# Optimization experiments

Measured on AMD Instinct MI355X. Metric: run time of the kernel, lower is better.

## Reference

```python
import jax, jax.numpy as jnp
import numpy as np

T, B, D, H, R, S, M = 1024, 16, 512, 8, 32, 16, 16
TQ = R + T + S   # query length
KL = M + R + T   # key/value length
NEG_INF = -1e8


def setup_inputs() -> dict:
    key = jax.random.key(0)
    ks = jax.random.split(key, 12)
    utterance = jax.random.normal(ks[0], (T, B, D), jnp.float32)
    right_context = jax.random.normal(ks[1], (R, B, D), jnp.float32)
    summary = jax.random.normal(ks[2], (S, B, D), jnp.float32)
    mems = jax.random.normal(ks[3], (M, B, D), jnp.float32)
    # valid lengths in [T//2, T]; force max == T so data-dependent shapes are static
    lengths = jax.random.randint(ks[4], (B,), T // 2, T + 1).at[0].set(T).astype(jnp.int64)
    # block-streaming style mask: query i may only attend to keys <= i + M
    q_idx = jnp.arange(TQ)[:, None]
    k_idx = jnp.arange(KL)[None, :]
    attention_mask = k_idx > (q_idx + M)  # True = masked
    scale = 0.02
    Wq = jax.random.normal(ks[5], (D, D), jnp.float32) * scale
    bq = jnp.zeros((D,), jnp.float32)
    Wkv = jax.random.normal(ks[6], (2 * D, D), jnp.float32) * scale
    bkv = jnp.zeros((2 * D,), jnp.float32)
    Wo = jax.random.normal(ks[7], (D, D), jnp.float32) * scale
    bo = jnp.zeros((D,), jnp.float32)
    return dict(utterance=utterance, lengths=lengths, right_context=right_context,
                summary=summary, mems=mems, attention_mask=attention_mask,
                Wq=Wq, bq=bq, Wkv=Wkv, bkv=bkv, Wo=Wo, bo=bo)


def _split_heads(x):
    # (L, B, D) -> (B*H, L, D//H), matching torch .view(-1, B*H, d).transpose(0, 1)
    L = x.shape[0]
    return x.reshape(L, B * H, D // H).transpose(1, 0, 2)


def reference(utterance, lengths, right_context, summary, mems, attention_mask,
              Wq, bq, Wkv, bkv, Wo, bo):
    d_head = D // H
    scaling = d_head ** -0.5

    query_in = jnp.concatenate([right_context, utterance, summary], axis=0)   # (TQ, B, D)
    kv_in = jnp.concatenate([mems, right_context, utterance], axis=0)         # (KL, B, D)

    query = query_in @ Wq.T + bq
    kv = kv_in @ Wkv.T + bkv
    k, v = jnp.split(kv, 2, axis=2)

    q = _split_heads(query)  # (B*H, TQ, d)
    kh = _split_heads(k)     # (B*H, KL, d)
    vh = _split_heads(v)

    w = jnp.einsum('nqd,nkd->nqk', q * scaling, kh).astype(jnp.float32)
    w = jnp.where(attention_mask[None, :, :], NEG_INF, w)

    # padding mask (B > 1 path): klengths = lengths + M + right_context_blocks_length
    rcbl = TQ - jnp.max(lengths) - S  # == R since max(lengths) == T
    klengths = lengths + M + rcbl
    pad_mask = jnp.arange(KL)[None, :] >= klengths[:, None]  # (B, KL)
    w = w.reshape(B, H, TQ, KL)
    w = jnp.where(pad_mask[:, None, None, :], NEG_INF, w)
    w = w.reshape(B * H, TQ, KL)

    probs = jax.nn.softmax(w, axis=-1)  # dropout p=0.0
    attn = jnp.einsum('nqk,nkd->nqd', probs, vh)          # (B*H, TQ, d)
    attn = attn.transpose(1, 0, 2).reshape(TQ, B, D)

    out = attn @ Wo.T + bo                                # (TQ, B, D)
    output_right_context = out[:TQ - S]                    # (R+T, B, D)
    output_mems = jnp.clip(out[TQ - S:], -10.0, 10.0)      # tanh_on_mem=False
    return output_right_context, output_mems[:-1]          # (S-1, B, D)
```

## Files before the change

kernel.cpp:

```cpp
#include <hip/hip_runtime.h>

#define T_   1024
#define B_   16
#define D_   512
#define H_   8
#define R_   32
#define S_   16
#define M_   16
#define TQ_  1072
#define KL_  1072
#define DH_  64
#define NROW 17152
#define K_   512
#define LQ_  268
#define QSCALE 0.18033688f

typedef unsigned short u16;
using bf16x8 = __attribute__((ext_vector_type(8))) short;
using f32x4  = __attribute__((ext_vector_type(4))) float;
using u16x4  = __attribute__((ext_vector_type(4))) unsigned short;

__device__ __forceinline__ u16 f2bf(float f) {
    unsigned int u = __builtin_bit_cast(unsigned int, f);
    unsigned int r = u + 0x7fffu + ((u >> 16) & 1u);
    return (u16)(r >> 16);
}

__device__ __forceinline__ void gload_lds16(const u16* g, u16* l) {
    __builtin_amdgcn_global_load_lds(
        (const __attribute__((address_space(1))) unsigned int*)g,
        (__attribute__((address_space(3))) unsigned int*)l,
        16, 0, 0);
}

__global__ void k_convert4(const float4* __restrict__ utt, const float4* __restrict__ rc,
                           const float4* __restrict__ smr, const float4* __restrict__ mems,
                           const float4* __restrict__ Wq, const float4* __restrict__ Wkv,
                           const float4* __restrict__ Wo,
                           u16x4* __restrict__ xall,
                           u16x4* __restrict__ wq, u16x4* __restrict__ wkv,
                           u16x4* __restrict__ wo)
{
    const int N4 = 17408 * D_ / 4;
    const int MB = M_ * B_ * D_ / 4;
    const int RB = MB + R_ * B_ * D_ / 4;
    const int UB = RB + T_ * B_ * D_ / 4;
    const int W1 = D_ * D_ / 4, W2 = 2 * D_ * D_ / 4;
    for (int i = blockIdx.x * blockDim.x + threadIdx.x; i < N4;
         i += gridDim.x * blockDim.x) {
        float4 v;
        if (i < MB)      v = mems[i];
        else if (i < RB) v = rc[i - MB];
        else if (i < UB) v = utt[i - RB];
        else             v = smr[i - UB];
        xall[i] = (u16x4){f2bf(v.x), f2bf(v.y), f2bf(v.z), f2bf(v.w)};
        if (i < W1) { v = Wq[i];  wq[i]  = (u16x4){f2bf(v.x), f2bf(v.y), f2bf(v.z), f2bf(v.w)}; }
        if (i < W2) { v = Wkv[i]; wkv[i] = (u16x4){f2bf(v.x), f2bf(v.y), f2bf(v.z), f2bf(v.w)}; }
        if (i < W1) { v = Wo[i];  wo[i]  = (u16x4){f2bf(v.x), f2bf(v.y), f2bf(v.z), f2bf(v.w)}; }
    }
}

__global__ __launch_bounds__(256, 2)
void k_gemm_qkv(const u16* __restrict__ xall,
                const u16* __restrict__ wqp, const u16* __restrict__ wkvp,
                const float* __restrict__ bq, const float* __restrict__ bkv,
                u16* __restrict__ qb, u16* __restrict__ kb, u16* __restrict__ vt)
{
    const int bid = blockIdx.x;
    const int tn = (bid % 96) >> 3;
    const int tm = (bid / 96) * 8 + (bid & 7);
    if (tm >= 134) return;

    __shared__ __align__(16) u16 As[128 * 32];
    __shared__ __align__(16) u16 Bs[128 * 32];

    const bool isQ = tn < 4;
    const int wr0 = (isQ ? tn : tn - 4) * 128;
    const u16* A = isQ ? (xall + (size_t)256 * K_) : xall;
    const u16* W = (isQ ? wqp : wkvp) + (size_t)wr0 * K_;
    const float* bias = isQ ? bq : bkv;

    const int w    = threadIdx.x >> 6;
    const int lane = threadIdx.x & 63;
    const int wm = w >> 1, wn = w & 1;
    const int col = lane & 15, quad = lane >> 4;

    const int srow = lane >> 2;
    const int skof = (lane & 3) * 8;
    const u16* gA = A + (size_t)(tm * 128 + w * 32 + srow) * K_ + skof;
    const u16* gW = W + (size_t)(w * 32 + srow) * K_ + skof;
    u16* lA = &As[(w * 32) * 32];
    u16* lB = &Bs[(w * 32) * 32];

    f32x4 acc[4][4];
#pragma unroll
    for (int mi = 0; mi < 4; mi++)
#pragma unroll
        for (int ni = 0; ni < 4; ni++) acc[mi][ni] = (f32x4){0.f, 0.f, 0.f, 0.f};

    for (int k0 = 0; k0 < K_; k0 += 32) {
        __syncthreads();
        gload_lds16(gA + k0,            lA);
        gload_lds16(gA + k0 + 16 * K_,  lA + 16 * 32);
        gload_lds16(gW + k0,            lB);
        gload_lds16(gW + k0 + 16 * K_,  lB + 16 * 32);
        __syncthreads();

        bf16x8 aF[4], bF[4];
#pragma unroll
        for (int mi = 0; mi < 4; mi++)
            aF[mi] = *(const bf16x8*)&As[(wm * 64 + mi * 16 + col) * 32 + quad * 8];
#pragma unroll
        for (int ni = 0; ni < 4; ni++)
            bF[ni] = *(const bf16x8*)&Bs[(wn * 64 + ni * 16 + col) * 32 + quad * 8];
#pragma unroll
        for (int mi = 0; mi < 4; mi++)
#pragma unroll
            for (int ni = 0; ni < 4; ni++)
                acc[mi][ni] = __builtin_amdgcn_mfma_f32_16x16x32_bf16(
                                  aF[mi], bF[ni], acc[mi][ni], 0, 0, 0);
    }

#pragma unroll
    for (int ni = 0; ni < 4; ni++) {
        int gcol = wr0 + wn * 64 + ni * 16 + col;
        float bs = bias[gcol];
        if (!isQ && gcol >= 512) {
            int f  = gcol - 512;
            int lq = tm * 2 + wm;
#pragma unroll
            for (int r = 0; r < 4; r++) {
                int bb = quad * 4 + r;
                u16x4 pk;
#pragma unroll
                for (int mi = 0; mi < 4; mi++)
                    pk[mi] = f2bf(acc[mi][ni][r] + bs);
                *(u16x4*)&vt[(((size_t)bb * LQ_ + lq) * 512 + f) * 4] = pk;
            }
            continue;
        }
#pragma unroll
        for (int mi = 0; mi < 4; mi++) {
#pragma unroll
            for (int r = 0; r < 4; r++) {
                int mrow = tm * 128 + wm * 64 + mi * 16 + quad * 4 + r;
                float val = acc[mi][ni][r] + bs;
                if (isQ) qb[(size_t)mrow * 512 + gcol] = f2bf(val * QSCALE);
                else     kb[(size_t)mrow * 512 + gcol] = f2bf(val);
            }
        }
    }
}

__global__ __launch_bounds__(256, 2)
void k_gemm_o(const u16* __restrict__ A, const u16* __restrict__ W,
              const float* __restrict__ bias, float* __restrict__ Co)
{
    const int bid = blockIdx.x;
    const int tn = (bid % 32) >> 3;
    const int tm = (bid / 32) * 8 + (bid & 7);
    if (tm >= 134) return;

    __shared__ __align__(16) u16 As[128 * 32];
    __shared__ __align__(16) u16 Bs[128 * 32];

    const int w    = threadIdx.x >> 6;
    const int lane = threadIdx.x & 63;
    const int wm = w >> 1, wn = w & 1;
    const int col = lane & 15, quad = lane >> 4;

    const int srow = lane >> 2;
    const int skof = (lane & 3) * 8;
    const u16* gA = A + (size_t)(tm * 128 + w * 32 + srow) * K_ + skof;
    const u16* gW = W + (size_t)(tn * 128 + w * 32 + srow) * K_ + skof;
    u16* lA = &As[(w * 32) * 32];
    u16* lB = &Bs[(w * 32) * 32];

    f32x4 acc[4][4];
#pragma unroll
    for (int mi = 0; mi < 4; mi++)
#pragma unroll
        for (int ni = 0; ni < 4; ni++) acc[mi][ni] = (f32x4){0.f, 0.f, 0.f, 0.f};

    for (int k0 = 0; k0 < K_; k0 += 32) {
        __syncthreads();
        gload_lds16(gA + k0,            lA);
        gload_lds16(gA + k0 + 16 * K_,  lA + 16 * 32);
        gload_lds16(gW + k0,            lB);
        gload_lds16(gW + k0 + 16 * K_,  lB + 16 * 32);
        __syncthreads();

        bf16x8 aF[4], bF[4];
#pragma unroll
        for (int mi = 0; mi < 4; mi++)
            aF[mi] = *(const bf16x8*)&As[(wm * 64 + mi * 16 + col) * 32 + quad * 8];
#pragma unroll
        for (int ni = 0; ni < 4; ni++)
            bF[ni] = *(const bf16x8*)&Bs[(wn * 64 + ni * 16 + col) * 32 + quad * 8];
#pragma unroll
        for (int mi = 0; mi < 4; mi++)
#pragma unroll
            for (int ni = 0; ni < 4; ni++)
                acc[mi][ni] = __builtin_amdgcn_mfma_f32_16x16x32_bf16(
                                  aF[mi], bF[ni], acc[mi][ni], 0, 0, 0);
    }

#pragma unroll
    for (int ni = 0; ni < 4; ni++) {
        int gcol = tn * 128 + wn * 64 + ni * 16 + col;
        float bs = bias[gcol];
#pragma unroll
        for (int mi = 0; mi < 4; mi++) {
#pragma unroll
            for (int r = 0; r < 4; r++) {
                int mrow = tm * 128 + wm * 64 + mi * 16 + quad * 4 + r;
                int l = mrow >> 4;
                if (l == TQ_ - 1) continue;
                float val = acc[mi][ni][r] + bs;
                if (l >= TQ_ - S_) val = fminf(10.0f, fmaxf(-10.0f, val));
                Co[(size_t)mrow * 512 + gcol] = val;
            }
        }
    }
}

__global__ __launch_bounds__(256, 2)
void k_attn4(const u16* __restrict__ qbuf, const u16* __restrict__ kb,
             const u16* __restrict__ vt, const int* __restrict__ lenp,
             u16* __restrict__ attnb)
{
    __shared__ __align__(16) u16 Ks[2][64 * 64];
    __shared__ __align__(16) u16 Vs[2][64 * 64];
    __shared__ __align__(16) u16 Ps[4][16 * 64];

    const int blk  = blockIdx.x;
    const int qblk = 16 - (blk >> 7);
    const int bh   = blk & 127;
    const int b = bh >> 3, h = bh & 7;
    const int tid = threadIdx.x;
    const int w = tid >> 6, lane = tid & 63;
    const int col = lane & 15, quad = lane >> 4;

    int stride = (lenp[1] == 0) ? 2 : 1;
    int maxlen = 0;
    for (int i = 0; i < B_; i++) maxlen = max(maxlen, lenp[i * stride]);
    const int klen = lenp[b * stride] + M_ + (TQ_ - maxlen - S_);

    const int q0 = qblk * 64;
    const int qw = q0 + w * 16;
    const int q  = qw + col;

    int qrow = min(q, TQ_ - 1);
    const u16* qp = qbuf + ((size_t)qrow * B_ + b) * D_ + h * DH_ + quad * 8;
    bf16x8 bq0 = *(const bf16x8*)(qp);
    bf16x8 bq1 = *(const bf16x8*)(qp + 32);

    const int s0 = tid, s1 = tid + 256;
    const u16* kbase = kb + (size_t)b * 512 + h * DH_;
    size_t kof0 = (size_t)(s0 >> 3) * 8192 + (size_t)(((s0 & 7) ^ ((s0 >> 3) & 7)) * 8);
    size_t kof1 = (size_t)(s1 >> 3) * 8192 + (size_t)(((s1 & 7) ^ ((s1 >> 3) & 7)) * 8);
    const u16* vbase = vt + ((size_t)b * LQ_ * 512 + (size_t)h * DH_) * 4;
    auto vchunk = [](int s) -> size_t {
        int fp = s >> 4;
        int lq = (s & 15) ^ (fp & 15);
        return (size_t)lq * 2048 + (size_t)fp * 8;
    };
    const size_t vof0 = vchunk(s0), vof1 = vchunk(s1);

    float mi = -1e30f, li = 0.f;
    f32x4 o[4];
#pragma unroll
    for (int g = 0; g < 4; g++) o[g] = (f32x4){0.f, 0.f, 0.f, 0.f};

    const int nk = min(q0 + 64 + M_, klen);
    const int numkt = (nk + 63) >> 6;
    u16* pw = &Ps[w][0];

    gload_lds16(kbase + kof0, &Ks[0][(size_t)w * 512]);
    gload_lds16(kbase + kof1, &Ks[0][2048 + (size_t)w * 512]);
    gload_lds16(vbase + vof0, &Vs[0][(size_t)w * 512]);
    gload_lds16(vbase + vof1, &Vs[0][2048 + (size_t)w * 512]);

    for (int kt = 0; kt < numkt; kt++) {
        const int kn0 = kt * 64;
        const int cur = kt & 1;
        __syncthreads();
        if (kt + 1 < numkt) {
            const size_t kstep = (size_t)(kn0 + 64) * 8192;
            const size_t vstep = (size_t)(kt + 1) * 32768;
            gload_lds16(kbase + kstep + kof0, &Ks[cur ^ 1][(size_t)w * 512]);
            gload_lds16(kbase + kstep + kof1, &Ks[cur ^ 1][2048 + (size_t)w * 512]);
            gload_lds16(vbase + vstep + vof0, &Vs[cur ^ 1][(size_t)w * 512]);
            gload_lds16(vbase + vstep + vof1, &Vs[cur ^ 1][2048 + (size_t)w * 512]);
        }

        f32x4 sc[4];
#pragma unroll
        for (int g = 0; g < 4; g++) {
            int key = g * 16 + col;
            bf16x8 a0 = *(const bf16x8*)&Ks[cur][key * 64 + ((quad ^ (key & 7)) * 8)];
            bf16x8 a1 = *(const bf16x8*)&Ks[cur][key * 64 + (((4 + quad) ^ (key & 7)) * 8)];
            f32x4 z = {0.f, 0.f, 0.f, 0.f};
            z = __builtin_amdgcn_mfma_f32_16x16x32_bf16(a0, bq0, z, 0, 0, 0);
            z = __builtin_amdgcn_mfma_f32_16x16x32_bf16(a1, bq1, z, 0, 0, 0);
            sc[g] = z;
        }

        const bool needmask = (kn0 + 63 > qw + M_) || (kn0 + 63 >= klen);
        if (needmask) {
#pragma unroll
            for (int g = 0; g < 4; g++)
#pragma unroll
                for (int r = 0; r < 4; r++) {
                    int key = kn0 + g * 16 + quad * 4 + r;
                    bool valid = (key <= q + M_) && (key < klen);
                    sc[g][r] = valid ? sc[g][r] : -1e8f;
                }
        }
        float mt = -1e30f;
#pragma unroll
        for (int g = 0; g < 4; g++)
#pragma unroll
            for (int r = 0; r < 4; r++) mt = fmaxf(mt, sc[g][r]);
        mt = fmaxf(mt, __shfl_xor(mt, 16));
        mt = fmaxf(mt, __shfl_xor(mt, 32));
        float mnew  = fmaxf(mi, mt);
        float alpha = __builtin_amdgcn_exp2f(mi - mnew);
        float sum = 0.f;
#pragma unroll
        for (int g = 0; g < 4; g++) {
            u16x4 pk;
#pragma unroll
            for (int r = 0; r < 4; r++) {
                float p = __builtin_amdgcn_exp2f(sc[g][r] - mnew);
                sum += p;
                pk[r] = f2bf(p);
            }
            int kc = g * 2 + (quad >> 1);
            *(u16x4*)&pw[col * 64 + ((kc ^ (col & 7)) * 8) + (quad & 1) * 4] = pk;
        }
        sum += __shfl_xor(sum, 16);
        sum += __shfl_xor(sum, 32);
        li = li * alpha + sum;
        mi = mnew;

#pragma unroll
        for (int r = 0; r < 4; r++) {
            float ar = __shfl(alpha, quad * 4 + r, 16);
#pragma unroll
            for (int g = 0; g < 4; g++) o[g][r] *= ar;
        }

        bf16x8 ap0 = *(const bf16x8*)&pw[col * 64 + ((quad ^ (col & 7)) * 8)];
        bf16x8 ap1 = *(const bf16x8*)&pw[col * 64 + (((4 + quad) ^ (col & 7)) * 8)];
#pragma unroll
        for (int g = 0; g < 4; g++) {
            int d = g * 16 + col;
            int fp = d >> 1, fo = (d & 1) * 4;
            bf16x8 bv[2];
#pragma unroll
            for (int hh = 0; hh < 2; hh++) {
                int lqA = hh * 8 + quad * 2;
                int posA = fp * 16 + (lqA ^ (fp & 15));
                int posB = fp * 16 + ((lqA + 1) ^ (fp & 15));
                u16x4 loA = *(const u16x4*)&Vs[cur][posA * 8 + fo];
                u16x4 loB = *(const u16x4*)&Vs[cur][posB * 8 + fo];
                bf16x8 t;
                t[0] = loA[0]; t[1] = loA[1]; t[2] = loA[2]; t[3] = loA[3];
                t[4] = loB[0]; t[5] = loB[1]; t[6] = loB[2]; t[7] = loB[3];
                bv[hh] = t;
            }
            o[g] = __builtin_amdgcn_mfma_f32_16x16x32_bf16(ap0, bv[0], o[g], 0, 0, 0);
            o[g] = __builtin_amdgcn_mfma_f32_16x16x32_bf16(ap1, bv[1], o[g], 0, 0, 0);
        }
    }

#pragma unroll
    for (int r = 0; r < 4; r++) {
        float lr = __shfl(li, quad * 4 + r, 16);
        float inv = 1.0f / lr;
        int qo = qw + quad * 4 + r;
        if (qo < TQ_) {
#pragma unroll
            for (int g = 0; g < 4; g++) {
                int d = h * DH_ + g * 16 + col;
                attnb[((size_t)qo * B_ + b) * D_ + d] = f2bf(o[g][r] * inv);
            }
        }
    }
}

extern "C" void kernel_launch(void* const* d_in, const int* in_sizes, int n_in,
                              void* d_out, int out_size, void* d_ws, size_t ws_size,
                              hipStream_t stream)
{
    const float* utt  = (const float*)d_in[0];
    const int*   len  = (const int*)  d_in[1];
    const float* rc   = (const float*)d_in[2];
    const float* smr  = (const float*)d_in[3];
    const float* mems = (const float*)d_in[4];
    const float* Wq   = (const float*)d_in[6];
    const float* bq   = (const float*)d_in[7];
    const float* Wkv  = (const float*)d_in[8];
    const float* bkv  = (const float*)d_in[9];
    const float* Wo   = (const float*)d_in[10];
    const float* bo   = (const float*)d_in[11];

    char* ws = (char*)d_ws;
    size_t off = 0;
    auto alloc = [&](size_t bytes) -> void* {
        void* p = ws + off;
        off += (bytes + 255) & ~(size_t)255;
        return p;
    };
    u16* xall = (u16*)alloc((size_t)17408 * D_ * 2);
    u16* wq   = (u16*)alloc((size_t)D_ * D_ * 2);
    u16* wkv  = (u16*)alloc((size_t)2 * D_ * D_ * 2);
    u16* wo   = (u16*)alloc((size_t)D_ * D_ * 2);
    u16* qb   = (u16*)alloc((size_t)NROW * D_ * 2);
    u16* kb   = (u16*)alloc((size_t)NROW * D_ * 2);
    u16* vt   = (u16*)alloc((size_t)B_ * LQ_ * 512 * 4 * 2 + 65536);
    u16* attnb = xall;

    k_convert4<<<2048, 256, 0, stream>>>((const float4*)utt, (const float4*)rc,
                                         (const float4*)smr, (const float4*)mems,
                                         (const float4*)Wq, (const float4*)Wkv,
                                         (const float4*)Wo,
                                         (u16x4*)xall,
                                         (u16x4*)wq, (u16x4*)wkv, (u16x4*)wo);
    k_gemm_qkv<<<17 * 96, 256, 0, stream>>>(xall, wq, wkv, bq, bkv, qb, kb, vt);
    k_attn4<<<17 * 128, 256, 0, stream>>>(qb, kb, vt, len, attnb);
    k_gemm_o<<<17 * 32, 256, 0, stream>>>(attnb, wo, bo, (float*)d_out);
}
```

Before: 219.4 us.

## Enlarge GEMM tiles to 256x128 with K=64 steps and XOR-swizzled LDS

Both projection GEMMs now use a shared core with 256x128 output tiles, a K-step of 64, and XOR-swizzled shared-memory chunks so fragment reads avoid bank conflicts. Each wave now owns a 64x128 slab (4x8 MFMA accumulators), which raises operand reuse and halves the number of K-loop barriers. The launch grids shrink to match. In exchange, register and LDS use per block grow (48KB LDS, 128 accumulator floats), which can lower occupancy, and the fewer, larger blocks may underfill the GPU's many CUs.

```diff
diff --git a/kernel.cpp b/kernel.cpp
--- a/kernel.cpp
+++ b/kernel.cpp
@@ -60,6 +60,52 @@
     }
 }
 
+#define GEMM_CORE(A_PTR, W_PTR)                                                  \
+    __shared__ __align__(16) u16 As[256 * 64];                                   \
+    __shared__ __align__(16) u16 Bs[128 * 64];                                   \
+    const int w    = threadIdx.x >> 6;                                           \
+    const int lane = threadIdx.x & 63;                                           \
+    const int col = lane & 15, quad = lane >> 4;                                 \
+    const int lrow = lane >> 3;                                        \
+    const int lchk = (lane & 7) ^ lrow;                      \
+    const u16* gA = (A_PTR) + (size_t)(tm * 256 + w * 64 + lrow) * K_ + lchk * 8;\
+    const u16* gB = (W_PTR) + (size_t)(w * 32 + lrow) * K_ + lchk * 8;           \
+    f32x4 acc[4][8];                                                             \
+    _Pragma("unroll")                                                            \
+    for (int mi = 0; mi < 4; mi++)                                               \
+        _Pragma("unroll")                                                        \
+        for (int ni = 0; ni < 8; ni++) acc[mi][ni] = (f32x4){0.f,0.f,0.f,0.f};   \
+    for (int k0 = 0; k0 < K_; k0 += 64) {                                        \
+        __syncthreads();                                                         \
+        _Pragma("unroll")                                                        \
+        for (int i = 0; i < 8; i++)                                              \
+            gload_lds16(gA + k0 + (size_t)i * 8 * K_,                            \
+                        &As[(w * 64 + i * 8) * 64]);                             \
+        _Pragma("unroll")                                                        \
+        for (int j = 0; j < 4; j++)                                              \
+            gload_lds16(gB + k0 + (size_t)j * 8 * K_,                            \
+                        &Bs[(w * 32 + j * 8) * 64]);                             \
+        __syncthreads();                                                         \
+        _Pragma("unroll")                                                        \
+        for (int kh = 0; kh < 2; kh++) {                                         \
+            bf16x8 aF[4], bF[8];                                                 \
+            _Pragma("unroll")                                                    \
+            for (int mi = 0; mi < 4; mi++)                                       \
+                aF[mi] = *(const bf16x8*)&As[(w * 64 + mi * 16 + col) * 64       \
+                             + (((kh * 4 + quad) ^ (col & 7)) * 8)];             \
+            _Pragma("unroll")                                                    \
+            for (int ni = 0; ni < 8; ni++)                                       \
+                bF[ni] = *(const bf16x8*)&Bs[(ni * 16 + col) * 64                \
+                             + (((kh * 4 + quad) ^ (col & 7)) * 8)];             \
+            _Pragma("unroll")                                                    \
+            for (int mi = 0; mi < 4; mi++)                                       \
+                _Pragma("unroll")                                                \
+                for (int ni = 0; ni < 8; ni++)                                   \
+                    acc[mi][ni] = __builtin_amdgcn_mfma_f32_16x16x32_bf16(       \
+                                      aF[mi], bF[ni], acc[mi][ni], 0, 0, 0);     \
+        }                                                                        \
+    }
+
 __global__ __launch_bounds__(256, 2)
 void k_gemm_qkv(const u16* __restrict__ xall,
                 const u16* __restrict__ wqp, const u16* __restrict__ wkvp,
@@ -69,65 +115,23 @@
     const int bid = blockIdx.x;
     const int tn = (bid % 96) >> 3;
     const int tm = (bid / 96) * 8 + (bid & 7);
-    if (tm >= 134) return;
-
-    __shared__ __align__(16) u16 As[128 * 32];
-    __shared__ __align__(16) u16 Bs[128 * 32];
+    if (tm >= 67) return;
 
     const bool isQ = tn < 4;
     const int wr0 = (isQ ? tn : tn - 4) * 128;
-    const u16* A = isQ ? (xall + (size_t)256 * K_) : xall;
-    const u16* W = (isQ ? wqp : wkvp) + (size_t)wr0 * K_;
+    const u16* Ab = isQ ? (xall + (size_t)256 * K_) : xall;
+    const u16* Wb = (isQ ? wqp : wkvp) + (size_t)wr0 * K_;
     const float* bias = isQ ? bq : bkv;
 
-    const int w    = threadIdx.x >> 6;
-    const int lane = threadIdx.x & 63;
-    const int wm = w >> 1, wn = w & 1;
-    const int col = lane & 15, quad = lane >> 4;
-
-    const int srow = lane >> 2;
-    const int skof = (lane & 3) * 8;
-    const u16* gA = A + (size_t)(tm * 128 + w * 32 + srow) * K_ + skof;
-    const u16* gW = W + (size_t)(w * 32 + srow) * K_ + skof;
-    u16* lA = &As[(w * 32) * 32];
-    u16* lB = &Bs[(w * 32) * 32];
-
-    f32x4 acc[4][4];
-#pragma unroll
-    for (int mi = 0; mi < 4; mi++)
-#pragma unroll
-        for (int ni = 0; ni < 4; ni++) acc[mi][ni] = (f32x4){0.f, 0.f, 0.f, 0.f};
-
-    for (int k0 = 0; k0 < K_; k0 += 32) {
-        __syncthreads();
-        gload_lds16(gA + k0,            lA);
-        gload_lds16(gA + k0 + 16 * K_,  lA + 16 * 32);
-        gload_lds16(gW + k0,            lB);
-        gload_lds16(gW + k0 + 16 * K_,  lB + 16 * 32);
-        __syncthreads();
-
-        bf16x8 aF[4], bF[4];
-#pragma unroll
-        for (int mi = 0; mi < 4; mi++)
-            aF[mi] = *(const bf16x8*)&As[(wm * 64 + mi * 16 + col) * 32 + quad * 8];
-#pragma unroll
-        for (int ni = 0; ni < 4; ni++)
-            bF[ni] = *(const bf16x8*)&Bs[(wn * 64 + ni * 16 + col) * 32 + quad * 8];
-#pragma unroll
-        for (int mi = 0; mi < 4; mi++)
-#pragma unroll
-            for (int ni = 0; ni < 4; ni++)
-                acc[mi][ni] = __builtin_amdgcn_mfma_f32_16x16x32_bf16(
-                                  aF[mi], bF[ni], acc[mi][ni], 0, 0, 0);
-    }
-
-#pragma unroll
-    for (int ni = 0; ni < 4; ni++) {
-        int gcol = wr0 + wn * 64 + ni * 16 + col;
+    GEMM_CORE(Ab, Wb)
+
+#pragma unroll
+    for (int ni = 0; ni < 8; ni++) {
+        int gcol = wr0 + ni * 16 + col;
         float bs = bias[gcol];
         if (!isQ && gcol >= 512) {
             int f  = gcol - 512;
-            int lq = tm * 2 + wm;
+            int lq = tm * 4 + w;
 #pragma unroll
             for (int r = 0; r < 4; r++) {
                 int bb = quad * 4 + r;
@@ -143,7 +147,7 @@
         for (int mi = 0; mi < 4; mi++) {
 #pragma unroll
             for (int r = 0; r < 4; r++) {
-                int mrow = tm * 128 + wm * 64 + mi * 16 + quad * 4 + r;
+                int mrow = tm * 256 + w * 64 + mi * 16 + quad * 4 + r;
                 float val = acc[mi][ni][r] + bs;
                 if (isQ) qb[(size_t)mrow * 512 + gcol] = f2bf(val * QSCALE);
                 else     kb[(size_t)mrow * 512 + gcol] = f2bf(val);
@@ -159,61 +163,21 @@
     const int bid = blockIdx.x;
     const int tn = (bid % 32) >> 3;
     const int tm = (bid / 32) * 8 + (bid & 7);
-    if (tm >= 134) return;
-
-    __shared__ __align__(16) u16 As[128 * 32];
-    __shared__ __align__(16) u16 Bs[128 * 32];
-
-    const int w    = threadIdx.x >> 6;
-    const int lane = threadIdx.x & 63;
-    const int wm = w >> 1, wn = w & 1;
-    const int col = lane & 15, quad = lane >> 4;
-
-    const int srow = lane >> 2;
-    const int skof = (lane & 3) * 8;
-    const u16* gA = A + (size_t)(tm * 128 + w * 32 + srow) * K_ + skof;
-    const u16* gW = W + (size_t)(tn * 128 + w * 32 + srow) * K_ + skof;
-    u16* lA = &As[(w * 32) * 32];
-    u16* lB = &Bs[(w * 32) * 32];
-
-    f32x4 acc[4][4];
-#pragma unroll
-    for (int mi = 0; mi < 4; mi++)
-#pragma unroll
-        for (int ni = 0; ni < 4; ni++) acc[mi][ni] = (f32x4){0.f, 0.f, 0.f, 0.f};
-
-    for (int k0 = 0; k0 < K_; k0 += 32) {
-        __syncthreads();
-        gload_lds16(gA + k0,            lA);
-        gload_lds16(gA + k0 + 16 * K_,  lA + 16 * 32);
-        gload_lds16(gW + k0,            lB);
-        gload_lds16(gW + k0 + 16 * K_,  lB + 16 * 32);
-        __syncthreads();
-
-        bf16x8 aF[4], bF[4];
-#pragma unroll
-        for (int mi = 0; mi < 4; mi++)
-            aF[mi] = *(const bf16x8*)&As[(wm * 64 + mi * 16 + col) * 32 + quad * 8];
-#pragma unroll
-        for (int ni = 0; ni < 4; ni++)
-            bF[ni] = *(const bf16x8*)&Bs[(wn * 64 + ni * 16 + col) * 32 + quad * 8];
-#pragma unroll
-        for (int mi = 0; mi < 4; mi++)
-#pragma unroll
-            for (int ni = 0; ni < 4; ni++)
-                acc[mi][ni] = __builtin_amdgcn_mfma_f32_16x16x32_bf16(
-                                  aF[mi], bF[ni], acc[mi][ni], 0, 0, 0);
-    }
-
-#pragma unroll
-    for (int ni = 0; ni < 4; ni++) {
-        int gcol = tn * 128 + wn * 64 + ni * 16 + col;
+    if (tm >= 67) return;
+
+    const u16* Wb = W + (size_t)tn * 128 * K_;
+
+    GEMM_CORE(A, Wb)
+
+#pragma unroll
+    for (int ni = 0; ni < 8; ni++) {
+        int gcol = tn * 128 + ni * 16 + col;
         float bs = bias[gcol];
 #pragma unroll
         for (int mi = 0; mi < 4; mi++) {
 #pragma unroll
             for (int r = 0; r < 4; r++) {
-                int mrow = tm * 128 + wm * 64 + mi * 16 + quad * 4 + r;
+                int mrow = tm * 256 + w * 64 + mi * 16 + quad * 4 + r;
                 int l = mrow >> 4;
                 if (l == TQ_ - 1) continue;
                 float val = acc[mi][ni][r] + bs;
@@ -428,7 +392,7 @@
                                          (const float4*)Wo,
                                          (u16x4*)xall,
                                          (u16x4*)wq, (u16x4*)wkv, (u16x4*)wo);
-    k_gemm_qkv<<<17 * 96, 256, 0, stream>>>(xall, wq, wkv, bq, bkv, qb, kb, vt);
+    k_gemm_qkv<<<9 * 96, 256, 0, stream>>>(xall, wq, wkv, bq, bkv, qb, kb, vt);
     k_attn4<<<17 * 128, 256, 0, stream>>>(qb, kb, vt, len, attnb);
-    k_gemm_o<<<17 * 32, 256, 0, stream>>>(attnb, wo, bo, (float*)d_out);
-}
+    k_gemm_o<<<9 * 32, 256, 0, stream>>>(attnb, wo, bo, (float*)d_out);
+}
```

Measured after the change: 217.8 us. No clear change (-0.7%).
